# Performance work log

Hardware: AMD Instinct MI355X
Metric: run time of the kernel (lower is better)

Reference implementation:

```python
import jax, jax.numpy as jnp
import numpy as np

TEMPERATURE = 0.05
EPS = 1e-8  # F.cosine_similarity default eps


def setup_inputs() -> dict:
    key = jax.random.key(0)
    k1, k2 = jax.random.split(key)
    N, D = 8192, 256
    return {
        "query_embeddings": jax.random.normal(k1, (N, D), dtype=jnp.float32),
        "pos_embeddings": jax.random.normal(k2, (N, D), dtype=jnp.float32),
    }


def _normalize(x):
    # matches F.cosine_similarity: x / max(||x||, eps)
    norm = jnp.sqrt(jnp.sum(x * x, axis=-1, keepdims=True))
    return x / jnp.maximum(norm, EPS)


def reference(query_embeddings, pos_embeddings):
    q = _normalize(query_embeddings)  # [N, D]
    p = _normalize(pos_embeddings)    # [N, D]
    # cosine similarity matrix via GEMM instead of (N,N,D) broadcast
    sim = jnp.einsum("nd,md->nm", q, p) / TEMPERATURE  # [N, N]
    # cross-entropy with labels = arange(N): loss_i = logsumexp(sim_i) - sim_ii
    logz = jax.nn.logsumexp(sim, axis=-1)  # [N]
    diag = jnp.diagonal(sim)               # [N]
    loss = jnp.mean(logz - diag)
    return loss
```

## Files before the change

kernel.cpp:

```cpp
#include <hip/hip_runtime.h>
#include <hip/hip_bf16.h>

#define NROWS 8192
#define DDIM  256
#define INV_TEMP 20.0f

typedef __attribute__((ext_vector_type(8)))  short bf16x8;
typedef __attribute__((ext_vector_type(16))) float f32x16;


__global__ __launch_bounds__(256) void norm_diag_kernel(
    const float* __restrict__ q, const float* __restrict__ p,
    unsigned short* __restrict__ qn, unsigned short* __restrict__ pn,
    float* __restrict__ diag, float* __restrict__ lse,
    unsigned int* __restrict__ counter)
{
    const int row  = blockIdx.x * 4 + (threadIdx.x >> 6);
    const int lane = threadIdx.x & 63;

    const float4 qv = ((const float4*)(q + (size_t)row * DDIM))[lane];
    const float4 pv = ((const float4*)(p + (size_t)row * DDIM))[lane];

    float sq = qv.x*qv.x + qv.y*qv.y + qv.z*qv.z + qv.w*qv.w;
    float sp = pv.x*pv.x + pv.y*pv.y + pv.z*pv.z + pv.w*pv.w;
    #pragma unroll
    for (int m = 1; m < 64; m <<= 1) {
        sq += __shfl_xor(sq, m);
        sp += __shfl_xor(sp, m);
    }
    const float qs = 1.0f / fmaxf(sqrtf(sq), 1e-8f);
    const float ps = 1.0f / fmaxf(sqrtf(sp), 1e-8f);

    const float qx = qv.x*qs, qy = qv.y*qs, qz = qv.z*qs, qw = qv.w*qs;
    const float px = pv.x*ps, py = pv.y*ps, pz = pv.z*ps, pw = pv.w*ps;

    float d = qx*px + qy*py + qz*pz + qw*pw;
    #pragma unroll
    for (int m = 1; m < 64; m <<= 1) d += __shfl_xor(d, m);
    if (lane == 0) {
        diag[row] = d * INV_TEMP;
        lse[row]  = 0.0f;
    }
    if (blockIdx.x == 0 && threadIdx.x == 0) *counter = 0u;

    union { unsigned short u16[4]; uint2 v; } uq, up;
    {
        __hip_bfloat16 b;
        b = __float2bfloat16(qx); uq.u16[0] = *(unsigned short*)&b;
        b = __float2bfloat16(qy); uq.u16[1] = *(unsigned short*)&b;
        b = __float2bfloat16(qz); uq.u16[2] = *(unsigned short*)&b;
        b = __float2bfloat16(qw); uq.u16[3] = *(unsigned short*)&b;
        b = __float2bfloat16(px); up.u16[0] = *(unsigned short*)&b;
        b = __float2bfloat16(py); up.u16[1] = *(unsigned short*)&b;
        b = __float2bfloat16(pz); up.u16[2] = *(unsigned short*)&b;
        b = __float2bfloat16(pw); up.u16[3] = *(unsigned short*)&b;
    }
    const int s = lane >> 2, h = (lane >> 1) & 1;
    const int cb = row >> 5, c = row & 31;
    const size_t dst = ((size_t)(s * 256 + cb) << 10) + (h << 9) + (c << 4)
                     + ((lane & 1) << 3);
    *(uint2*)((char*)qn + dst) = uq.v;
    *(uint2*)((char*)pn + dst) = up.v;
}

__global__ __launch_bounds__(256, 2) void simexp_kernel(
    const unsigned short* __restrict__ qn,
    const unsigned short* __restrict__ pn,
    float* __restrict__ lse, const float* __restrict__ diag,
    unsigned int* __restrict__ counter, float* __restrict__ out)
{
    __shared__ float wsum[4];
    __shared__ unsigned int is_last;

    const int tid  = threadIdx.x;
    const int lane = tid & 63;
    const int w    = tid >> 6;
    const int rowstart = blockIdx.y * 256 + w * 64;
    const int cbA = rowstart >> 5;
    const int cb0 = blockIdx.x * 16;

    bf16x8 a0[16], a1[16];
    #pragma unroll
    for (int s = 0; s < 16; ++s) {
        a0[s] = *(const bf16x8*)(qn + (size_t)(s * 256 + cbA    ) * 512 + lane * 8);
        a1[s] = *(const bf16x8*)(qn + (size_t)(s * 256 + cbA + 1) * 512 + lane * 8);
    }

    const unsigned short* bbase = pn + lane * 8;
    #define FRAG(f) (*(const bf16x8*)(bbase + \
        (size_t)((((f) & 15) * 256) + cb0 + ((f) >> 4)) * 512))

    bf16x8 bq[4] = { FRAG(0), FRAG(1), FRAG(2), FRAG(3) };

    f32x16 lsum0 = (f32x16)0.0f, lsum1 = (f32x16)0.0f;

    for (int c = 0; c < 16; ++c) {
        f32x16 acc0 = (f32x16)0.0f, acc1 = (f32x16)0.0f;
        #pragma unroll
        for (int s = 0; s < 16; ++s) {
            bf16x8 cur = bq[s & 3];
            const int f = c * 16 + s + 4;
            if (f < 256) bq[s & 3] = FRAG(f);
            acc0 = __builtin_amdgcn_mfma_f32_32x32x16_bf16(a0[s], cur, acc0, 0, 0, 0);
            acc1 = __builtin_amdgcn_mfma_f32_32x32x16_bf16(a1[s], cur, acc1, 0, 0, 0);
        }
        #pragma unroll
        for (int r = 0; r < 16; ++r) {
            lsum0[r] += __expf(acc0[r] * INV_TEMP);
            lsum1[r] += __expf(acc1[r] * INV_TEMP);
        }
    }
    #undef FRAG

    #pragma unroll
    for (int r = 0; r < 16; ++r) {
        float v0 = lsum0[r], v1 = lsum1[r];
        #pragma unroll
        for (int m = 1; m < 32; m <<= 1) {
            v0 += __shfl_xor(v0, m);
            v1 += __shfl_xor(v1, m);
        }
        if ((lane & 31) == 0) {
            const int rl = (r & 3) + 8 * (r >> 2) + ((lane >> 5) << 2);
            atomicAdd(&lse[rowstart + rl],      v0);
            atomicAdd(&lse[rowstart + 32 + rl], v1);
        }
    }

    __threadfence();
    __syncthreads();
    if (tid == 0) {
        const unsigned int nblk = gridDim.x * gridDim.y;
        is_last = (atomicAdd(counter, 1u) == nblk - 1u);
    }
    __syncthreads();
    if (is_last) {
        __threadfence();
        float s = 0.0f;
        for (int i = tid; i < NROWS; i += 256) {
            float v = __hip_atomic_load(&lse[i], __ATOMIC_RELAXED,
                                        __HIP_MEMORY_SCOPE_AGENT);
            s += __logf(v) - diag[i];
        }
        #pragma unroll
        for (int m = 1; m < 64; m <<= 1) s += __shfl_xor(s, m);
        if (lane == 0) wsum[w] = s;
        __syncthreads();
        if (tid == 0)
            out[0] = (wsum[0] + wsum[1] + wsum[2] + wsum[3]) * (1.0f / NROWS);
    }
}

extern "C" void kernel_launch(void* const* d_in, const int* in_sizes, int n_in,
                              void* d_out, int out_size, void* d_ws, size_t ws_size,
                              hipStream_t stream)
{
    const float* q = (const float*)d_in[0];
    const float* p = (const float*)d_in[1];

    char* ws = (char*)d_ws;
    unsigned short* qn = (unsigned short*)ws;
    unsigned short* pn = (unsigned short*)(ws + (size_t)NROWS*DDIM*2);
    float* diag = (float*)(ws + 2 * (size_t)NROWS * DDIM * 2);
    float* lse  = diag + NROWS;
    unsigned int* counter = (unsigned int*)(lse + NROWS);

    norm_diag_kernel<<<NROWS / 4, 256, 0, stream>>>(q, p, qn, pn, diag, lse, counter);

    dim3 grid(16, 32);
    simexp_kernel<<<grid, 256, 0, stream>>>(qn, pn, lse, diag, counter, (float*)d_out);
}
```

Measured before the change: 151.0 us.

## Halve per-wave row tile, deepen B prefetch, raise occupancy to three blocks

Each wave now computes one 32-row block instead of two. That frees the second A fragment set and accumulator, so launch bounds can request 3 blocks per CU and the grid doubles along rows. The B-fragment prefetch ring grows from 4 to 8 entries to hide more load latency. The cost is that each B fragment now feeds only one MFMA instead of two, which doubles B global/L2 traffic per FLOP. The loop also loads past the last fragment without a bounds guard, reading beyond the intended region at the tail.

Result: slower. 177.1 us (+17.3%).

```diff
diff --git a/kernel.cpp b/kernel.cpp
--- a/kernel.cpp
+++ b/kernel.cpp
@@ -63,7 +63,7 @@
     *(uint2*)((char*)pn + dst) = up.v;
 }
 
-__global__ __launch_bounds__(256, 2) void simexp_kernel(
+__global__ __launch_bounds__(256, 3) void simexp_kernel(
     const unsigned short* __restrict__ qn,
     const unsigned short* __restrict__ pn,
     float* __restrict__ lse, const float* __restrict__ diag,
@@ -75,55 +75,47 @@
     const int tid  = threadIdx.x;
     const int lane = tid & 63;
     const int w    = tid >> 6;
-    const int rowstart = blockIdx.y * 256 + w * 64;
-    const int cbA = rowstart >> 5;
+    const int rowstart = blockIdx.y * 128 + w * 32;
+    const int cbA = blockIdx.y * 4 + w;
     const int cb0 = blockIdx.x * 16;
 
-    bf16x8 a0[16], a1[16];
+    bf16x8 a[16];
     #pragma unroll
-    for (int s = 0; s < 16; ++s) {
-        a0[s] = *(const bf16x8*)(qn + (size_t)(s * 256 + cbA    ) * 512 + lane * 8);
-        a1[s] = *(const bf16x8*)(qn + (size_t)(s * 256 + cbA + 1) * 512 + lane * 8);
-    }
+    for (int s = 0; s < 16; ++s)
+        a[s] = *(const bf16x8*)(qn + ((size_t)(s * 256 + cbA) << 9) + lane * 8);
 
     const unsigned short* bbase = pn + lane * 8;
     #define FRAG(f) (*(const bf16x8*)(bbase + \
-        (size_t)((((f) & 15) * 256) + cb0 + ((f) >> 4)) * 512))
+        ((size_t)((((f) & 15) << 8) + cb0 + ((f) >> 4)) << 9)))
 
-    bf16x8 bq[4] = { FRAG(0), FRAG(1), FRAG(2), FRAG(3) };
+    bf16x8 bq[8];
+    #pragma unroll
+    for (int i = 0; i < 8; ++i) bq[i] = FRAG(i);
 
-    f32x16 lsum0 = (f32x16)0.0f, lsum1 = (f32x16)0.0f;
+    f32x16 lsum = (f32x16)0.0f;
 
-    for (int c = 0; c < 16; ++c) {
-        f32x16 acc0 = (f32x16)0.0f, acc1 = (f32x16)0.0f;
+    for (int cbi = 0; cbi < 16; ++cbi) {
+        f32x16 acc = (f32x16)0.0f;
         #pragma unroll
         for (int s = 0; s < 16; ++s) {
-            bf16x8 cur = bq[s & 3];
-            const int f = c * 16 + s + 4;
-            if (f < 256) bq[s & 3] = FRAG(f);
-            acc0 = __builtin_amdgcn_mfma_f32_32x32x16_bf16(a0[s], cur, acc0, 0, 0, 0);
-            acc1 = __builtin_amdgcn_mfma_f32_32x32x16_bf16(a1[s], cur, acc1, 0, 0, 0);
+            acc = __builtin_amdgcn_mfma_f32_32x32x16_bf16(a[s], bq[s & 7], acc, 0, 0, 0);
+            const int fn = cbi * 16 + s + 8;
+            bq[s & 7] = FRAG(fn);
         }
         #pragma unroll
-        for (int r = 0; r < 16; ++r) {
-            lsum0[r] += __expf(acc0[r] * INV_TEMP);
-            lsum1[r] += __expf(acc1[r] * INV_TEMP);
-        }
+        for (int r = 0; r < 16; ++r)
+            lsum[r] += __expf(acc[r] * INV_TEMP);
     }
     #undef FRAG
 
     #pragma unroll
     for (int r = 0; r < 16; ++r) {
-        float v0 = lsum0[r], v1 = lsum1[r];
+        float v = lsum[r];
         #pragma unroll
-        for (int m = 1; m < 32; m <<= 1) {
-            v0 += __shfl_xor(v0, m);
-            v1 += __shfl_xor(v1, m);
-        }
+        for (int m = 1; m < 32; m <<= 1) v += __shfl_xor(v, m);
         if ((lane & 31) == 0) {
             const int rl = (r & 3) + 8 * (r >> 2) + ((lane >> 5) << 2);
-            atomicAdd(&lse[rowstart + rl],      v0);
-            atomicAdd(&lse[rowstart + 32 + rl], v1);
+            atomicAdd(&lse[rowstart + rl], v);
         }
     }
 
@@ -167,6 +159,6 @@
 
     norm_diag_kernel<<<NROWS / 4, 256, 0, stream>>>(q, p, qn, pn, diag, lse, counter);
 
-    dim3 grid(16, 32);
+    dim3 grid(16, 64);
     simexp_kernel<<<grid, 256, 0, stream>>>(qn, pn, lse, diag, counter, (float*)d_out);
 }
```
